# Optimization experiments

Measured on AMD Instinct MI355X. Metric: run time of the kernel, lower is better.

## Reference

```python
import jax, jax.numpy as jnp
import numpy as np

K = 10          # number of neighbors (init kwarg k)
NUM_CLASSES = 100  # label vocabulary (targets drawn in [0, 100))


def setup_inputs() -> dict:
    key = jax.random.key(0)
    k1, k2, k3 = jax.random.split(key, 3)
    X = jax.random.normal(k1, (1024, 512), dtype=jnp.float32)
    data = jax.random.normal(k2, (50000, 512), dtype=jnp.float32)
    targets = jax.random.randint(k3, (50000,), 0, NUM_CLASSES, dtype=jnp.int64)
    return {"X": X, "data": data, "targets": targets}


def reference(X, data, targets):
    # Pairwise L2 distance (p=2 path of the module), computed via the
    x2 = jnp.sum(X * X, axis=1, keepdims=True)              # [Q, 1]
    d2 = jnp.sum(data * data, axis=1)                        # [N]
    sq = x2 + d2[None, :] - 2.0 * (X @ data.T)               # [Q, N]
    dist = jnp.sqrt(jnp.maximum(sq, 0.0))                    # torch.norm(p1-p2, p=2)

    # torch: sort distances ascending, take first k indices -> top-k smallest.
    _, idx = jax.lax.top_k(-dist, K)                         # [Q, K]
    labels = targets[idx]                                    # [Q, K]

    # torch.mode over the k neighbor labels: histogram + argmax.
    # argmax picks the first (smallest) class on ties, matching torch.mode.
    counts = jax.nn.one_hot(labels, NUM_CLASSES, dtype=jnp.float32).sum(axis=1)  # [Q, C]
    pred = jnp.argmax(counts, axis=1).astype(jnp.float32)    # [Q]
    return pred
```

## Files before the change

kernel.cpp:

```cpp
#include <hip/hip_runtime.h>
#include <math.h>
#include <limits.h>

#define QN 1024
#define NN 50000
#define NPAD 50048
#define DD 512
#define KNN 10
#define NT 128
#define QTB 128
#define BK 32
#define NS 391
#define QB 8
#define NSAMP 31
#define NREST (NS - NSAMP)
#define CAP 512
#define SLACK 4.0f
#define LCAP 1152

#define WS_D2  0
#define WS_TAU 50048
#define WS_CNT (WS_TAU + 1024)
#define WS_XH  (WS_CNT + 1024)
#define WS_CKS (WS_XH + QN * DD / 2)
#define WS_BUF (WS_CKS + QN * NSAMP * KNN * 2)
#define WS_DH  (WS_BUF + QN * CAP * 2)
#define WS_END (WS_DH + NS * 16 * 2048)

typedef __attribute__((ext_vector_type(8))) short short8;
typedef __attribute__((ext_vector_type(4))) float f32x4;
typedef unsigned long long u64;

__device__ __forceinline__ u64 mkkey(float f, int idx) {
  unsigned u = __float_as_uint(f);
  unsigned m = u ^ ((unsigned)((int)u >> 31) | 0x80000000u);
  return ((u64)m << 32) | (unsigned)idx;
}

__device__ __forceinline__ float keyhi_f(unsigned m) {
  unsigned u = (m & 0x80000000u) ? (m ^ 0x80000000u) : ~m;
  return __uint_as_float(u);
}

__device__ __forceinline__ unsigned cvth(float x, float y) {
  unsigned ux = __float_as_uint(x), uy = __float_as_uint(y);
  unsigned rx = ux + 0x7fffu + ((ux >> 16) & 1u);
  unsigned ry = uy + 0x7fffu + ((uy >> 16) & 1u);
  return (rx >> 16) | (ry & 0xffff0000u);
}

__device__ __forceinline__ void glds16(const void* g, void* l) {
  __builtin_amdgcn_global_load_lds(
      (const __attribute__((address_space(1))) unsigned*)g,
      (__attribute__((address_space(3))) unsigned*)l, 16, 0, 0);
}

__device__ __forceinline__ void ins10(u64* kl, u64 k) {
#pragma unroll
  for (int u = 0; u < KNN; u++) {
    u64 lo = (k < kl[u]) ? k : kl[u];
    u64 hi = (k < kl[u]) ? kl[u] : k;
    kl[u] = lo; k = hi;
  }
}

__global__ __launch_bounds__(256) void conv_kernel(
    const float* __restrict__ dat, const float* __restrict__ Xm,
    float* __restrict__ ws) {
  if ((int)blockIdx.x >= NS) {
    const int g = ((int)blockIdx.x - NS) * 256 + threadIdx.x;
    const int b = g >> 10, kc = (g >> 6) & 15, l = g & 63;
    const int row = b * 16 + (l & 15);
    const int col = kc * 32 + (l >> 4) * 8;
    const float4* p = (const float4*)(Xm + (size_t)row * DD + col);
    float4 v0 = p[0], v1 = p[1];
    ((uint4*)(ws + WS_XH))[g] = make_uint4(
        cvth(v0.x, v0.y), cvth(v0.z, v0.w), cvth(v1.x, v1.y), cvth(v1.z, v1.w));
    return;
  }
  const int slice = blockIdx.x;
  const int t = threadIdx.x;
  const int row = t >> 1, h2 = t & 1;
  const int gr = slice * NT + row;
  const int r15 = row & 15;
  float s = 0.f;
#pragma unroll
  for (int kc8 = 0; kc8 < 8; kc8++) {
    const int kc = h2 * 8 + kc8;
    float4 v[8];
    if (gr < NN) {
      const float4* src = (const float4*)(dat + (size_t)gr * DD + kc * 32);
#pragma unroll
      for (int j = 0; j < 8; j++) v[j] = src[j];
    } else {
#pragma unroll
      for (int j = 0; j < 8; j++) v[j] = make_float4(0.f, 0.f, 0.f, 0.f);
    }
    unsigned hw[16];
#pragma unroll
    for (int j = 0; j < 8; j++) {
      s = fmaf(v[j].x, v[j].x, s); s = fmaf(v[j].y, v[j].y, s);
      s = fmaf(v[j].z, v[j].z, s); s = fmaf(v[j].w, v[j].w, s);
      hw[2 * j]     = cvth(v[j].x, v[j].y);
      hw[2 * j + 1] = cvth(v[j].z, v[j].w);
    }
    uint4* dhp = (uint4*)((unsigned char*)(ws + WS_DH) +
                          (((size_t)slice * 16 + kc) * 8 + (row >> 4)) * 1024);
#pragma unroll
    for (int qd = 0; qd < 4; qd++)
      dhp[qd * 16 + r15] = make_uint4(hw[4 * qd], hw[4 * qd + 1], hw[4 * qd + 2], hw[4 * qd + 3]);
  }
  s += __shfl_xor(s, 1, 64);
  if (h2 == 0) ws[WS_D2 + gr] = (gr < NN) ? s : __builtin_inff();
}

struct StageT { unsigned char ah[8192], bh[8192]; };
struct EpiT  { float sq[64][132]; };
struct ListT { u64 kl[64][4][KNN]; };

template <int MODE> struct SmemSel {
  union U { StageT s; EpiT e; ListT l; };
};
template <> struct SmemSel<1> {
  struct U { StageT s; float tau[128]; };
};

template <int PRE, int MODE>
__global__ __launch_bounds__(256, 3) void knn_chunk(
    const float* __restrict__ dat, float* __restrict__ ws, int soff) {
  __shared__ __align__(16) typename SmemSel<MODE>::U sm;
  int bqx, bsy;
  if (MODE == 1 && (gridDim.y & 7) == 0) {
    const int n = (int)(blockIdx.y * gridDim.x + blockIdx.x);
    const int m = n >> 3;
    const int ypx = (int)(gridDim.y >> 3);
    bqx = m & 7;
    bsy = (n & 7) * ypx + (m >> 3);
  } else {
    bqx = blockIdx.x; bsy = blockIdx.y;
  }
  const int qbase = bqx * QTB;
  const int slice = bsy + soff;
  const int nbase = slice * NT;
  const int t = threadIdx.x;
  const int lane = t & 63, wave = t >> 6;
  const int wn = wave & 1, wq = wave >> 1;
  const unsigned char* dh = (const unsigned char*)(ws + WS_DH);
  const char* xfh = (const char*)(ws + WS_XH);

  f32x4 acc[4][4];
#pragma unroll
  for (int i = 0; i < 4; i++)
#pragma unroll
    for (int j = 0; j < 4; j++) acc[i][j] = (f32x4)0.f;

  auto stage = [&](int kc) {
#pragma unroll
    for (int i = 0; i < 2; i++) {
      int pp = wave * 2 + i;
      const char* ga = xfh +
          ((((size_t)(bqx * 8 + pp) * 16 + kc) * 64) + lane) * 16;
      glds16(ga, sm.s.ah + pp * 1024);
    }
#pragma unroll
    for (int i = 0; i < 2; i++) {
      int p = wave * 2 + i;
      const unsigned char* gb = dh +
          (((size_t)slice * 16 + kc) * 8 + p) * 1024 + lane * 16;
      glds16(gb, sm.s.bh + p * 1024);
    }
  };

  if (PRE) {
    stage(0);
    for (int kc = 0; kc < 16; kc++) {
      __syncthreads();
      const int fragoff = lane * 16;
      short8 fah[4], fbh[4];
#pragma unroll
      for (int i = 0; i < 4; i++) {
        fah[i] = *(const short8*)(sm.s.ah + (wq * 4 + i) * 1024 + fragoff);
        fbh[i] = *(const short8*)(sm.s.bh + (wn * 4 + i) * 1024 + fragoff);
      }
      __syncthreads();
      if (kc < 15) stage(kc + 1);
#pragma unroll
      for (int mt = 0; mt < 4; mt++)
#pragma unroll
        for (int nt = 0; nt < 4; nt++)
          acc[mt][nt] = __builtin_amdgcn_mfma_f32_16x16x32_bf16(fah[mt], fbh[nt], acc[mt][nt], 0, 0, 0);
    }
  } else {
    const int abase = (((bqx * 8 + wq * 4) * 16) * 64 + lane) * 16;
    const int brow = t >> 1, bh_half = t & 1;
    const int bgr = nbase + brow;
    const int bpanel = (brow >> 4) * 1024;
    const int bchunk = (brow & 15) * 16;
    for (int kc = 0; kc < 16; kc++) {
      const int kk = kc * BK;
      short8 fah[4];
#pragma unroll
      for (int i = 0; i < 4; i++)
        fah[i] = *(const short8*)(xfh + abase + i * 16384 + kc * 1024);
      __syncthreads();
      {
        float4 v0 = make_float4(0.f, 0.f, 0.f, 0.f), v1 = v0, v2 = v0, v3 = v0;
        if (bgr < NN) {
          const float4* src = (const float4*)(dat + (size_t)bgr * DD + kk + bh_half * 16);
          v0 = src[0]; v1 = src[1]; v2 = src[2]; v3 = src[3];
        }
        unsigned char* bhp = sm.s.bh + bpanel;
        *(uint4*)(bhp + (2 * bh_half) * 256 + bchunk) =
            make_uint4(cvth(v0.x, v0.y), cvth(v0.z, v0.w), cvth(v1.x, v1.y), cvth(v1.z, v1.w));
        *(uint4*)(bhp + (2 * bh_half + 1) * 256 + bchunk) =
            make_uint4(cvth(v2.x, v2.y), cvth(v2.z, v2.w), cvth(v3.x, v3.y), cvth(v3.z, v3.w));
      }
      __syncthreads();
      const int fragoff = lane * 16;
      short8 fbh[4];
#pragma unroll
      for (int i = 0; i < 4; i++)
        fbh[i] = *(const short8*)(sm.s.bh + (wn * 4 + i) * 1024 + fragoff);
      __syncthreads();
#pragma unroll
      for (int mt = 0; mt < 4; mt++)
#pragma unroll
        for (int nt = 0; nt < 4; nt++)
          acc[mt][nt] = __builtin_amdgcn_mfma_f32_16x16x32_bf16(fah[mt], fbh[nt], acc[mt][nt], 0, 0, 0);
    }
  }

  if constexpr (MODE == 0) {
#pragma unroll
    for (int pass = 0; pass < 2; pass++) {
      __syncthreads();
      if (wq == pass) {
#pragma unroll
        for (int nt = 0; nt < 4; nt++) {
          int col = wn * 64 + nt * 16 + (lane & 15);
          float d2v = ws[WS_D2 + nbase + col];
#pragma unroll
          for (int mt = 0; mt < 4; mt++)
#pragma unroll
            for (int rg = 0; rg < 4; rg++) {
              int lr = mt * 16 + (lane >> 4) * 4 + rg;
              sm.e.sq[lr][col] = fmaf(-2.f, acc[mt][nt][rg], d2v);
            }
        }
      }
      __syncthreads();
      {
        const int r = t >> 2, s = t & 3;
        u64 kl[KNN];
#pragma unroll
        for (int u = 0; u < KNN; u++) kl[u] = ~0ull;
        for (int jj = 0; jj < 32; jj++) {
          int c = s * 32 + ((jj + r + 8 * s) & 31);
          float v = sm.e.sq[r][c];
          ins10(kl, mkkey(v, nbase + c));
        }
        __syncthreads();
#pragma unroll
        for (int u = 0; u < KNN; u++) sm.l.kl[r][s][u] = kl[u];
      }
      __syncthreads();
      if (t < 64) {
        u64* dst = ((u64*)(ws + WS_CKS)) +
                   ((size_t)(qbase + pass * 64 + t) * NSAMP + blockIdx.y) * KNN;
        int h0 = 0, h1 = 0, h2 = 0, h3 = 0;
        for (int pick = 0; pick < KNN; pick++) {
          u64 k0 = sm.l.kl[t][0][h0], k1 = sm.l.kl[t][1][h1];
          u64 k2 = sm.l.kl[t][2][h2], k3 = sm.l.kl[t][3][h3];
          u64 best = k0; int bm = 0;
          if (k1 < best) { best = k1; bm = 1; }
          if (k2 < best) { best = k2; bm = 2; }
          if (k3 < best) { best = k3; bm = 3; }
          dst[pick] = best;
          h0 += (bm == 0); h1 += (bm == 1); h2 += (bm == 2); h3 += (bm == 3);
        }
      }
    }
  } else {
    if (t < 128) sm.tau[t] = ws[WS_TAU + qbase + t];
    __syncthreads();
    unsigned* cnt = (unsigned*)(ws + WS_CNT);
    u64* buf = (u64*)(ws + WS_BUF);
    float d2v[4];
#pragma unroll
    for (int nt = 0; nt < 4; nt++)
      d2v[nt] = ws[WS_D2 + nbase + wn * 64 + nt * 16 + (lane & 15)];
#pragma unroll
    for (int mt = 0; mt < 4; mt++)
#pragma unroll
      for (int rg = 0; rg < 4; rg++) {
        int row = wq * 64 + mt * 16 + (lane >> 4) * 4 + rg;
        float tr = sm.tau[row];
#pragma unroll
        for (int nt = 0; nt < 4; nt++) {
          float d = fmaf(-2.f, acc[mt][nt][rg], d2v[nt]);
          if (d < tr) {
            int col = nbase + wn * 64 + nt * 16 + (lane & 15);
            int q = qbase + row;
            unsigned slot = atomicAdd(cnt + q, 1u);
            if (slot < CAP) buf[(size_t)q * CAP + slot] = mkkey(d, col);
          }
        }
      }
  }
}

__global__ __launch_bounds__(64) void tau_kernel(float* __restrict__ ws) {
  const int q = blockIdx.x;
  const int t = threadIdx.x;
  const u64* samp = ((const u64*)(ws + WS_CKS)) + (size_t)q * NSAMP * KNN;
  const int NC = NSAMP * KNN;
  u64 kl[KNN];
#pragma unroll
  for (int u = 0; u < KNN; u++) kl[u] = ~0ull;
  for (int j = t; j < NC; j += 64) ins10(kl, samp[j]);
  __shared__ u64 wk[64][KNN];
  __shared__ u64 m2[8][KNN];
#pragma unroll
  for (int u = 0; u < KNN; u++) wk[t][u] = kl[u];
  __syncthreads();
  if (t < 8) {
    int h[8] = {0, 0, 0, 0, 0, 0, 0, 0};
    for (int pick = 0; pick < KNN; pick++) {
      u64 best = ~0ull; int bm = 0;
#pragma unroll
      for (int m = 0; m < 8; m++) {
        u64 km = wk[t * 8 + m][h[m]];
        if (km < best) { best = km; bm = m; }
      }
      m2[t][pick] = best;
#pragma unroll
      for (int m = 0; m < 8; m++) h[m] += (bm == m);
    }
  }
  __syncthreads();
  if (t == 0) {
    int h[8] = {0, 0, 0, 0, 0, 0, 0, 0};
    u64 best = 0;
    for (int pick = 0; pick < KNN; pick++) {
      best = ~0ull; int bm = 0;
#pragma unroll
      for (int m = 0; m < 8; m++) {
        u64 km = m2[m][h[m]];
        if (km < best) { best = km; bm = m; }
      }
#pragma unroll
      for (int m = 0; m < 8; m++) h[m] += (bm == m);
    }
    ws[WS_TAU + q] = keyhi_f((unsigned)(best >> 32)) + SLACK;
    ((unsigned*)(ws + WS_CNT))[q] = 0u;
  }
}

__global__ __launch_bounds__(256) void knn_final(
    const int* __restrict__ targets, const float* __restrict__ Xm,
    const float* __restrict__ dat, float* __restrict__ ws,
    float* __restrict__ out) {
  const int q = blockIdx.x;
  const int t = threadIdx.x;
  const int lane = t & 63, wave = t >> 6;
  __shared__ float qrow[DD];
  __shared__ unsigned lst[LCAP];
  __shared__ int nlist;
  __shared__ u64 wk4[4][KNN];
  if (t == 0) nlist = 0;
  if (t < 128) ((float4*)qrow)[t] = ((const float4*)(Xm + (size_t)q * DD))[t];
  __syncthreads();
  const float tr = ws[WS_TAU + q];
  const u64* samp = ((const u64*)(ws + WS_CKS)) + (size_t)q * NSAMP * KNN;
  for (int j = t; j < NSAMP * KNN; j += 256) {
    u64 k = samp[j];
    if (keyhi_f((unsigned)(k >> 32)) < tr) {
      int s_ = atomicAdd(&nlist, 1);
      if (s_ < LCAP) lst[s_] = (unsigned)k;
    }
  }
  unsigned c = ((const unsigned*)(ws + WS_CNT))[q];
  if (c > CAP) c = CAP;
  const u64* buf = ((const u64*)(ws + WS_BUF)) + (size_t)q * CAP;
  for (int j = t; j < (int)c; j += 256) {
    int s_ = atomicAdd(&nlist, 1);
    if (s_ < LCAP) lst[s_] = (unsigned)buf[j];
  }
  __syncthreads();
  const int n = nlist < LCAP ? nlist : LCAP;

  u64 kl[KNN];
#pragma unroll
  for (int u = 0; u < KNN; u++) kl[u] = ~0ull;
  const float4* qv = (const float4*)qrow;
  const float4 q0 = qv[lane * 2], q1 = qv[lane * 2 + 1];
  for (int j = wave; j < n; j += 8) {
    const unsigned i0 = lst[j];
    const int has1 = (j + 4) < n;
    const unsigned i1 = has1 ? lst[j + 4] : i0;
    const float4* x0 = (const float4*)(dat + (size_t)i0 * DD) + lane * 2;
    const float4* x1 = (const float4*)(dat + (size_t)i1 * DD) + lane * 2;
    const float4 a0 = x0[0], a1 = x0[1];
    const float4 b0 = x1[0], b1 = x1[1];
    float p0 = a0.x * q0.x, p1 = b0.x * q0.x;
    p0 = fmaf(a0.y, q0.y, p0); p1 = fmaf(b0.y, q0.y, p1);
    p0 = fmaf(a0.z, q0.z, p0); p1 = fmaf(b0.z, q0.z, p1);
    p0 = fmaf(a0.w, q0.w, p0); p1 = fmaf(b0.w, q0.w, p1);
    p0 = fmaf(a1.x, q1.x, p0); p1 = fmaf(b1.x, q1.x, p1);
    p0 = fmaf(a1.y, q1.y, p0); p1 = fmaf(b1.y, q1.y, p1);
    p0 = fmaf(a1.z, q1.z, p0); p1 = fmaf(b1.z, q1.z, p1);
    p0 = fmaf(a1.w, q1.w, p0); p1 = fmaf(b1.w, q1.w, p1);
#pragma unroll
    for (int s_ = 1; s_ < 64; s_ <<= 1) {
      p0 += __shfl_xor(p0, s_, 64);
      p1 += __shfl_xor(p1, s_, 64);
    }
    float d0 = fmaf(-2.f, p0, ws[WS_D2 + i0]);
    u64 k0 = mkkey(d0, (int)i0);
    if (k0 < kl[KNN - 1]) ins10(kl, k0);
    if (has1) {
      float d1 = fmaf(-2.f, p1, ws[WS_D2 + i1]);
      u64 k1 = mkkey(d1, (int)i1);
      if (k1 < kl[KNN - 1]) ins10(kl, k1);
    }
  }
  if (lane == 0)
#pragma unroll
    for (int u = 0; u < KNN; u++) wk4[wave][u] = kl[u];
  __syncthreads();
  if (t == 0) {
    int h[4] = {0, 0, 0, 0};
    int fi[KNN];
    for (int pick = 0; pick < KNN; pick++) {
      u64 best = ~0ull; int bm = 0;
#pragma unroll
      for (int m = 0; m < 4; m++) {
        u64 km = wk4[m][h[m]];
        if (km < best) { best = km; bm = m; }
      }
      fi[pick] = (int)(unsigned)(best & 0xffffffffu);
      h[bm]++;
    }
    int lab[KNN];
#pragma unroll
    for (int u = 0; u < KNN; u++) lab[u] = targets[fi[u]];
    int bc = 0, bl = INT_MAX;
#pragma unroll
    for (int i = 0; i < KNN; i++) {
      int cc = 0;
#pragma unroll
      for (int j = 0; j < KNN; j++) cc += (lab[j] == lab[i]) ? 1 : 0;
      if (cc > bc || (cc == bc && lab[i] < bl)) { bc = cc; bl = lab[i]; }
    }
    out[q] = (float)bl;
  }
}

extern "C" void kernel_launch(void* const* d_in, const int* in_sizes, int n_in,
                              void* d_out, int out_size, void* d_ws, size_t ws_size,
                              hipStream_t stream) {
  const float* Xm  = (const float*)d_in[0];
  const float* dat = (const float*)d_in[1];
  const int* targets = (const int*)d_in[2];
  float* out = (float*)d_out;
  float* ws  = (float*)d_ws;
  const bool pre = ws_size >= (size_t)WS_END * 4;

  hipLaunchKernelGGL(conv_kernel, dim3(NS + QN * DD / 8 / 256), dim3(256), 0,
                     stream, dat, Xm, ws);
  if (pre) {
    hipLaunchKernelGGL((knn_chunk<1, 0>), dim3(QB, NSAMP), dim3(256), 0, stream, dat, ws, 0);
    hipLaunchKernelGGL(tau_kernel, dim3(QN), dim3(64), 0, stream, ws);
    hipLaunchKernelGGL((knn_chunk<1, 1>), dim3(QB, NREST), dim3(256), 0, stream, dat, ws, NSAMP);
  } else {
    hipLaunchKernelGGL((knn_chunk<0, 0>), dim3(QB, NSAMP), dim3(256), 0, stream, dat, ws, 0);
    hipLaunchKernelGGL(tau_kernel, dim3(QN), dim3(64), 0, stream, ws);
    hipLaunchKernelGGL((knn_chunk<0, 1>), dim3(QB, NREST), dim3(256), 0, stream, dat, ws, NSAMP);
  }
  hipLaunchKernelGGL(knn_final, dim3(QN), dim3(256), 0, stream, targets, Xm, dat, ws, out);
}
```

Baseline: 335.2 us.

## Fuse conversion and sample top-k into one kernel, enlarge sample set

Merges the fp32-to-bf16 conversion kernel and the sampling top-k kernel into one launch. The sampling blocks now load fp32 data directly, convert X and data in registers and compute norms inline, while the other blocks convert only the remaining slices. The sample slice count doubles from 31 to 63 to tighten the threshold for the filter pass. The workspace-size fallback path is dropped, so the large workspace is always assumed. The cost is more sample-phase work and uncoalesced fp32 reads of X in the sampling blocks, in exchange for one fewer launch and a tighter threshold that should mean fewer filter candidates.

```diff
diff --git a/kernel.cpp b/kernel.cpp
--- a/kernel.cpp
+++ b/kernel.cpp
@@ -12,7 +12,7 @@
 #define BK 32
 #define NS 391
 #define QB 8
-#define NSAMP 31
+#define NSAMP 63
 #define NREST (NS - NSAMP)
 #define CAP 512
 #define SLACK 4.0f
@@ -64,11 +64,21 @@
   }
 }
 
-__global__ __launch_bounds__(256) void conv_kernel(
+struct EpiT  { float sq[64][132]; };
+struct ListT { u64 kl[64][4][KNN]; };
+struct Smem0 {
+  union { unsigned char bh[8192]; EpiT e; ListT l; } u;
+  float d2loc[128];
+};
+
+__global__ __launch_bounds__(256, 3) void fused_kernel(
     const float* __restrict__ dat, const float* __restrict__ Xm,
     float* __restrict__ ws) {
-  if ((int)blockIdx.x >= NS) {
-    const int g = ((int)blockIdx.x - NS) * 256 + threadIdx.x;
+  const int bid = (int)blockIdx.x;
+  const int t = threadIdx.x;
+
+  if (bid >= QB * NSAMP + NREST) {
+    const int g = (bid - (QB * NSAMP + NREST)) * 256 + t;
     const int b = g >> 10, kc = (g >> 6) & 15, l = g & 63;
     const int row = b * 16 + (l & 15);
     const int col = kc * 32 + (l >> 4) * 8;
@@ -78,75 +88,189 @@
         cvth(v0.x, v0.y), cvth(v0.z, v0.w), cvth(v1.x, v1.y), cvth(v1.z, v1.w));
     return;
   }
-  const int slice = blockIdx.x;
-  const int t = threadIdx.x;
-  const int row = t >> 1, h2 = t & 1;
-  const int gr = slice * NT + row;
-  const int r15 = row & 15;
+
+  if (bid >= QB * NSAMP) {
+    const int slice = NSAMP + (bid - QB * NSAMP);
+    const int row = t >> 1, h2 = t & 1;
+    const int gr = slice * NT + row;
+    const int r15 = row & 15;
+    float s = 0.f;
+#pragma unroll
+    for (int kc8 = 0; kc8 < 8; kc8++) {
+      const int kc = h2 * 8 + kc8;
+      float4 v[8];
+      if (gr < NN) {
+        const float4* src = (const float4*)(dat + (size_t)gr * DD + kc * 32);
+#pragma unroll
+        for (int j = 0; j < 8; j++) v[j] = src[j];
+      } else {
+#pragma unroll
+        for (int j = 0; j < 8; j++) v[j] = make_float4(0.f, 0.f, 0.f, 0.f);
+      }
+      unsigned hw[16];
+#pragma unroll
+      for (int j = 0; j < 8; j++) {
+        s = fmaf(v[j].x, v[j].x, s); s = fmaf(v[j].y, v[j].y, s);
+        s = fmaf(v[j].z, v[j].z, s); s = fmaf(v[j].w, v[j].w, s);
+        hw[2 * j]     = cvth(v[j].x, v[j].y);
+        hw[2 * j + 1] = cvth(v[j].z, v[j].w);
+      }
+      uint4* dhp = (uint4*)((unsigned char*)(ws + WS_DH) +
+                            (((size_t)slice * 16 + kc) * 8 + (row >> 4)) * 1024);
+#pragma unroll
+      for (int qd = 0; qd < 4; qd++)
+        dhp[qd * 16 + r15] = make_uint4(hw[4 * qd], hw[4 * qd + 1], hw[4 * qd + 2], hw[4 * qd + 3]);
+    }
+    s += __shfl_xor(s, 1, 64);
+    if (h2 == 0) ws[WS_D2 + gr] = (gr < NN) ? s : __builtin_inff();
+    return;
+  }
+
+  __shared__ __align__(16) Smem0 sm;
+  const int m = bid;
+  const int bqx = m & 7;
+  const int bsy = m >> 3;
+  const int qbase = bqx * QTB;
+  const int slice = bsy;
+  const int nbase = slice * NT;
+  const int lane = t & 63, wave = t >> 6;
+  const int wn = wave & 1, wq = wave >> 1;
+
+  f32x4 acc[4][4];
+#pragma unroll
+  for (int i = 0; i < 4; i++)
+#pragma unroll
+    for (int j = 0; j < 4; j++) acc[i][j] = (f32x4)0.f;
+
+  const int brow = t >> 1, bh_half = t & 1;
+  const int bgr = nbase + brow;
+  const int bpanel = (brow >> 4) * 1024;
+  const int bchunk = (brow & 15) * 16;
   float s = 0.f;
-#pragma unroll
-  for (int kc8 = 0; kc8 < 8; kc8++) {
-    const int kc = h2 * 8 + kc8;
-    float4 v[8];
-    if (gr < NN) {
-      const float4* src = (const float4*)(dat + (size_t)gr * DD + kc * 32);
-#pragma unroll
-      for (int j = 0; j < 8; j++) v[j] = src[j];
-    } else {
-#pragma unroll
-      for (int j = 0; j < 8; j++) v[j] = make_float4(0.f, 0.f, 0.f, 0.f);
-    }
-    unsigned hw[16];
-#pragma unroll
-    for (int j = 0; j < 8; j++) {
-      s = fmaf(v[j].x, v[j].x, s); s = fmaf(v[j].y, v[j].y, s);
-      s = fmaf(v[j].z, v[j].z, s); s = fmaf(v[j].w, v[j].w, s);
-      hw[2 * j]     = cvth(v[j].x, v[j].y);
-      hw[2 * j + 1] = cvth(v[j].z, v[j].w);
-    }
-    uint4* dhp = (uint4*)((unsigned char*)(ws + WS_DH) +
-                          (((size_t)slice * 16 + kc) * 8 + (row >> 4)) * 1024);
-#pragma unroll
-    for (int qd = 0; qd < 4; qd++)
-      dhp[qd * 16 + r15] = make_uint4(hw[4 * qd], hw[4 * qd + 1], hw[4 * qd + 2], hw[4 * qd + 3]);
+  for (int kc = 0; kc < 16; kc++) {
+    const int kk = kc * BK;
+    short8 fah[4];
+#pragma unroll
+    for (int i = 0; i < 4; i++) {
+      const int p = wq * 4 + i;
+      const float4* xr = (const float4*)(
+          Xm + (size_t)(qbase + p * 16 + (lane & 15)) * DD + kk + (lane >> 4) * 8);
+      float4 v0 = xr[0], v1 = xr[1];
+      union { unsigned w[4]; short8 s8; } pk;
+      pk.w[0] = cvth(v0.x, v0.y); pk.w[1] = cvth(v0.z, v0.w);
+      pk.w[2] = cvth(v1.x, v1.y); pk.w[3] = cvth(v1.z, v1.w);
+      fah[i] = pk.s8;
+    }
+    __syncthreads();
+    {
+      float4 v0 = make_float4(0.f, 0.f, 0.f, 0.f), v1 = v0, v2 = v0, v3 = v0;
+      if (bgr < NN) {
+        const float4* src = (const float4*)(dat + (size_t)bgr * DD + kk + bh_half * 16);
+        v0 = src[0]; v1 = src[1]; v2 = src[2]; v3 = src[3];
+      }
+      s = fmaf(v0.x, v0.x, s); s = fmaf(v0.y, v0.y, s);
+      s = fmaf(v0.z, v0.z, s); s = fmaf(v0.w, v0.w, s);
+      s = fmaf(v1.x, v1.x, s); s = fmaf(v1.y, v1.y, s);
+      s = fmaf(v1.z, v1.z, s); s = fmaf(v1.w, v1.w, s);
+      s = fmaf(v2.x, v2.x, s); s = fmaf(v2.y, v2.y, s);
+      s = fmaf(v2.z, v2.z, s); s = fmaf(v2.w, v2.w, s);
+      s = fmaf(v3.x, v3.x, s); s = fmaf(v3.y, v3.y, s);
+      s = fmaf(v3.z, v3.z, s); s = fmaf(v3.w, v3.w, s);
+      uint4 q0 = make_uint4(cvth(v0.x, v0.y), cvth(v0.z, v0.w), cvth(v1.x, v1.y), cvth(v1.z, v1.w));
+      uint4 q1 = make_uint4(cvth(v2.x, v2.y), cvth(v2.z, v2.w), cvth(v3.x, v3.y), cvth(v3.z, v3.w));
+      unsigned char* bhp = sm.u.bh + bpanel;
+      *(uint4*)(bhp + (2 * bh_half) * 256 + bchunk)     = q0;
+      *(uint4*)(bhp + (2 * bh_half + 1) * 256 + bchunk) = q1;
+    }
+    __syncthreads();
+    const int fragoff = lane * 16;
+    short8 fbh[4];
+#pragma unroll
+    for (int i = 0; i < 4; i++)
+      fbh[i] = *(const short8*)(sm.u.bh + (wn * 4 + i) * 1024 + fragoff);
+    __syncthreads();
+#pragma unroll
+    for (int mt = 0; mt < 4; mt++)
+#pragma unroll
+      for (int nt = 0; nt < 4; nt++)
+        acc[mt][nt] = __builtin_amdgcn_mfma_f32_16x16x32_bf16(fah[mt], fbh[nt], acc[mt][nt], 0, 0, 0);
   }
   s += __shfl_xor(s, 1, 64);
-  if (h2 == 0) ws[WS_D2 + gr] = (gr < NN) ? s : __builtin_inff();
-}
-
-struct StageT { unsigned char ah[8192], bh[8192]; };
-struct EpiT  { float sq[64][132]; };
-struct ListT { u64 kl[64][4][KNN]; };
-
-template <int MODE> struct SmemSel {
-  union U { StageT s; EpiT e; ListT l; };
-};
-template <> struct SmemSel<1> {
-  struct U { StageT s; float tau[128]; };
-};
-
-template <int PRE, int MODE>
-__global__ __launch_bounds__(256, 3) void knn_chunk(
-    const float* __restrict__ dat, float* __restrict__ ws, int soff) {
-  __shared__ __align__(16) typename SmemSel<MODE>::U sm;
-  int bqx, bsy;
-  if (MODE == 1 && (gridDim.y & 7) == 0) {
-    const int n = (int)(blockIdx.y * gridDim.x + blockIdx.x);
-    const int m = n >> 3;
-    const int ypx = (int)(gridDim.y >> 3);
-    bqx = m & 7;
-    bsy = (n & 7) * ypx + (m >> 3);
-  } else {
-    bqx = blockIdx.x; bsy = blockIdx.y;
-  }
+  if (bh_half == 0) {
+    sm.d2loc[brow] = s;
+    ws[WS_D2 + bgr] = s;
+  }
+
+#pragma unroll
+  for (int pass = 0; pass < 2; pass++) {
+    __syncthreads();
+    if (wq == pass) {
+#pragma unroll
+      for (int nt = 0; nt < 4; nt++) {
+        int col = wn * 64 + nt * 16 + (lane & 15);
+        float d2v = sm.d2loc[col];
+#pragma unroll
+        for (int mt = 0; mt < 4; mt++)
+#pragma unroll
+          for (int rg = 0; rg < 4; rg++) {
+            int lr = mt * 16 + (lane >> 4) * 4 + rg;
+            sm.u.e.sq[lr][col] = fmaf(-2.f, acc[mt][nt][rg], d2v);
+          }
+      }
+    }
+    __syncthreads();
+    {
+      const int r = t >> 2, s4 = t & 3;
+      u64 kl[KNN];
+#pragma unroll
+      for (int u = 0; u < KNN; u++) kl[u] = ~0ull;
+      for (int jj = 0; jj < 32; jj++) {
+        int c = s4 * 32 + ((jj + r + 8 * s4) & 31);
+        float v = sm.u.e.sq[r][c];
+        ins10(kl, mkkey(v, nbase + c));
+      }
+      __syncthreads();
+#pragma unroll
+      for (int u = 0; u < KNN; u++) sm.u.l.kl[r][s4][u] = kl[u];
+    }
+    __syncthreads();
+    if (t < 64) {
+      u64* dst = ((u64*)(ws + WS_CKS)) +
+                 ((size_t)(qbase + pass * 64 + t) * NSAMP + bsy) * KNN;
+      int h0 = 0, h1 = 0, h2c = 0, h3 = 0;
+      for (int pick = 0; pick < KNN; pick++) {
+        u64 k0 = sm.u.l.kl[t][0][h0], k1 = sm.u.l.kl[t][1][h1];
+        u64 k2 = sm.u.l.kl[t][2][h2c], k3 = sm.u.l.kl[t][3][h3];
+        u64 best = k0; int bm = 0;
+        if (k1 < best) { best = k1; bm = 1; }
+        if (k2 < best) { best = k2; bm = 2; }
+        if (k3 < best) { best = k3; bm = 3; }
+        dst[pick] = best;
+        h0 += (bm == 0); h1 += (bm == 1); h2c += (bm == 2); h3 += (bm == 3);
+      }
+    }
+  }
+}
+
+struct SmemF { unsigned char bh[8192]; float tau[128]; };
+
+__global__ __launch_bounds__(256, 3) void knn_filter(
+    float* __restrict__ ws) {
+  __shared__ __align__(16) SmemF sm;
+  const int n = (int)(blockIdx.y * gridDim.x + blockIdx.x);
+  const int mm = n >> 3;
+  const int ypx = (int)(gridDim.y >> 3);
+  const int bqx = mm & 7;
+  const int bsy = (n & 7) * ypx + (mm >> 3);
   const int qbase = bqx * QTB;
-  const int slice = bsy + soff;
+  const int slice = bsy + NSAMP;
   const int nbase = slice * NT;
   const int t = threadIdx.x;
   const int lane = t & 63, wave = t >> 6;
   const int wn = wave & 1, wq = wave >> 1;
   const unsigned char* dh = (const unsigned char*)(ws + WS_DH);
   const char* xfh = (const char*)(ws + WS_XH);
+  const int abase = (((bqx * 8 + wq * 4) * 16) * 64 + lane) * 16;
 
   f32x4 acc[4][4];
 #pragma unroll
@@ -154,159 +278,62 @@
 #pragma unroll
     for (int j = 0; j < 4; j++) acc[i][j] = (f32x4)0.f;
 
-  auto stage = [&](int kc) {
-#pragma unroll
-    for (int i = 0; i < 2; i++) {
-      int pp = wave * 2 + i;
-      const char* ga = xfh +
-          ((((size_t)(bqx * 8 + pp) * 16 + kc) * 64) + lane) * 16;
-      glds16(ga, sm.s.ah + pp * 1024);
-    }
+  auto stageB = [&](int kc) {
 #pragma unroll
     for (int i = 0; i < 2; i++) {
       int p = wave * 2 + i;
-      const unsigned char* gb = dh +
+      const unsigned char* g = dh +
           (((size_t)slice * 16 + kc) * 8 + p) * 1024 + lane * 16;
-      glds16(gb, sm.s.bh + p * 1024);
+      glds16(g, sm.bh + p * 1024);
     }
   };
 
-  if (PRE) {
-    stage(0);
-    for (int kc = 0; kc < 16; kc++) {
-      __syncthreads();
-      const int fragoff = lane * 16;
-      short8 fah[4], fbh[4];
-#pragma unroll
-      for (int i = 0; i < 4; i++) {
-        fah[i] = *(const short8*)(sm.s.ah + (wq * 4 + i) * 1024 + fragoff);
-        fbh[i] = *(const short8*)(sm.s.bh + (wn * 4 + i) * 1024 + fragoff);
-      }
-      __syncthreads();
-      if (kc < 15) stage(kc + 1);
-#pragma unroll
-      for (int mt = 0; mt < 4; mt++)
-#pragma unroll
-        for (int nt = 0; nt < 4; nt++)
-          acc[mt][nt] = __builtin_amdgcn_mfma_f32_16x16x32_bf16(fah[mt], fbh[nt], acc[mt][nt], 0, 0, 0);
-    }
-  } else {
-    const int abase = (((bqx * 8 + wq * 4) * 16) * 64 + lane) * 16;
-    const int brow = t >> 1, bh_half = t & 1;
-    const int bgr = nbase + brow;
-    const int bpanel = (brow >> 4) * 1024;
-    const int bchunk = (brow & 15) * 16;
-    for (int kc = 0; kc < 16; kc++) {
-      const int kk = kc * BK;
-      short8 fah[4];
-#pragma unroll
-      for (int i = 0; i < 4; i++)
-        fah[i] = *(const short8*)(xfh + abase + i * 16384 + kc * 1024);
-      __syncthreads();
-      {
-        float4 v0 = make_float4(0.f, 0.f, 0.f, 0.f), v1 = v0, v2 = v0, v3 = v0;
-        if (bgr < NN) {
-          const float4* src = (const float4*)(dat + (size_t)bgr * DD + kk + bh_half * 16);
-          v0 = src[0]; v1 = src[1]; v2 = src[2]; v3 = src[3];
+  stageB(0);
+  for (int kc = 0; kc < 16; kc++) {
+    short8 fah[4];
+#pragma unroll
+    for (int i = 0; i < 4; i++)
+      fah[i] = *(const short8*)(xfh + abase + i * 16384 + kc * 1024);
+    __syncthreads();
+    const int fragoff = lane * 16;
+    short8 fbh[4];
+#pragma unroll
+    for (int i = 0; i < 4; i++)
+      fbh[i] = *(const short8*)(sm.bh + (wn * 4 + i) * 1024 + fragoff);
+    __syncthreads();
+    if (kc < 15) stageB(kc + 1);
+#pragma unroll
+    for (int mt = 0; mt < 4; mt++)
+#pragma unroll
+      for (int nt = 0; nt < 4; nt++)
+        acc[mt][nt] = __builtin_amdgcn_mfma_f32_16x16x32_bf16(fah[mt], fbh[nt], acc[mt][nt], 0, 0, 0);
+  }
+
+  if (t < 128) sm.tau[t] = ws[WS_TAU + qbase + t];
+  __syncthreads();
+  unsigned* cnt = (unsigned*)(ws + WS_CNT);
+  u64* buf = (u64*)(ws + WS_BUF);
+  float d2v[4];
+#pragma unroll
+  for (int nt = 0; nt < 4; nt++)
+    d2v[nt] = ws[WS_D2 + nbase + wn * 64 + nt * 16 + (lane & 15)];
+#pragma unroll
+  for (int mt = 0; mt < 4; mt++)
+#pragma unroll
+    for (int rg = 0; rg < 4; rg++) {
+      int row = wq * 64 + mt * 16 + (lane >> 4) * 4 + rg;
+      float tr = sm.tau[row];
+#pragma unroll
+      for (int nt = 0; nt < 4; nt++) {
+        float d = fmaf(-2.f, acc[mt][nt][rg], d2v[nt]);
+        if (d < tr) {
+          int col = nbase + wn * 64 + nt * 16 + (lane & 15);
+          int q = qbase + row;
+          unsigned slot = atomicAdd(cnt + q, 1u);
+          if (slot < CAP) buf[(size_t)q * CAP + slot] = mkkey(d, col);
         }
-        unsigned char* bhp = sm.s.bh + bpanel;
-        *(uint4*)(bhp + (2 * bh_half) * 256 + bchunk) =
-            make_uint4(cvth(v0.x, v0.y), cvth(v0.z, v0.w), cvth(v1.x, v1.y), cvth(v1.z, v1.w));
-        *(uint4*)(bhp + (2 * bh_half + 1) * 256 + bchunk) =
-            make_uint4(cvth(v2.x, v2.y), cvth(v2.z, v2.w), cvth(v3.x, v3.y), cvth(v3.z, v3.w));
-      }
-      __syncthreads();
-      const int fragoff = lane * 16;
-      short8 fbh[4];
-#pragma unroll
-      for (int i = 0; i < 4; i++)
-        fbh[i] = *(const short8*)(sm.s.bh + (wn * 4 + i) * 1024 + fragoff);
-      __syncthreads();
-#pragma unroll
-      for (int mt = 0; mt < 4; mt++)
-#pragma unroll
-        for (int nt = 0; nt < 4; nt++)
-          acc[mt][nt] = __builtin_amdgcn_mfma_f32_16x16x32_bf16(fah[mt], fbh[nt], acc[mt][nt], 0, 0, 0);
-    }
-  }
-
-  if constexpr (MODE == 0) {
-#pragma unroll
-    for (int pass = 0; pass < 2; pass++) {
-      __syncthreads();
-      if (wq == pass) {
-#pragma unroll
-        for (int nt = 0; nt < 4; nt++) {
-          int col = wn * 64 + nt * 16 + (lane & 15);
-          float d2v = ws[WS_D2 + nbase + col];
-#pragma unroll
-          for (int mt = 0; mt < 4; mt++)
-#pragma unroll
-            for (int rg = 0; rg < 4; rg++) {
-              int lr = mt * 16 + (lane >> 4) * 4 + rg;
-              sm.e.sq[lr][col] = fmaf(-2.f, acc[mt][nt][rg], d2v);
-            }
-        }
-      }
-      __syncthreads();
-      {
-        const int r = t >> 2, s = t & 3;
-        u64 kl[KNN];
-#pragma unroll
-        for (int u = 0; u < KNN; u++) kl[u] = ~0ull;
-        for (int jj = 0; jj < 32; jj++) {
-          int c = s * 32 + ((jj + r + 8 * s) & 31);
-          float v = sm.e.sq[r][c];
-          ins10(kl, mkkey(v, nbase + c));
-        }
-        __syncthreads();
-#pragma unroll
-        for (int u = 0; u < KNN; u++) sm.l.kl[r][s][u] = kl[u];
-      }
-      __syncthreads();
-      if (t < 64) {
-        u64* dst = ((u64*)(ws + WS_CKS)) +
-                   ((size_t)(qbase + pass * 64 + t) * NSAMP + blockIdx.y) * KNN;
-        int h0 = 0, h1 = 0, h2 = 0, h3 = 0;
-        for (int pick = 0; pick < KNN; pick++) {
-          u64 k0 = sm.l.kl[t][0][h0], k1 = sm.l.kl[t][1][h1];
-          u64 k2 = sm.l.kl[t][2][h2], k3 = sm.l.kl[t][3][h3];
-          u64 best = k0; int bm = 0;
-          if (k1 < best) { best = k1; bm = 1; }
-          if (k2 < best) { best = k2; bm = 2; }
-          if (k3 < best) { best = k3; bm = 3; }
-          dst[pick] = best;
-          h0 += (bm == 0); h1 += (bm == 1); h2 += (bm == 2); h3 += (bm == 3);
-        }
-      }
-    }
-  } else {
-    if (t < 128) sm.tau[t] = ws[WS_TAU + qbase + t];
-    __syncthreads();
-    unsigned* cnt = (unsigned*)(ws + WS_CNT);
-    u64* buf = (u64*)(ws + WS_BUF);
-    float d2v[4];
-#pragma unroll
-    for (int nt = 0; nt < 4; nt++)
-      d2v[nt] = ws[WS_D2 + nbase + wn * 64 + nt * 16 + (lane & 15)];
-#pragma unroll
-    for (int mt = 0; mt < 4; mt++)
-#pragma unroll
-      for (int rg = 0; rg < 4; rg++) {
-        int row = wq * 64 + mt * 16 + (lane >> 4) * 4 + rg;
-        float tr = sm.tau[row];
-#pragma unroll
-        for (int nt = 0; nt < 4; nt++) {
-          float d = fmaf(-2.f, acc[mt][nt][rg], d2v[nt]);
-          if (d < tr) {
-            int col = nbase + wn * 64 + nt * 16 + (lane & 15);
-            int q = qbase + row;
-            unsigned slot = atomicAdd(cnt + q, 1u);
-            if (slot < CAP) buf[(size_t)q * CAP + slot] = mkkey(d, col);
-          }
-        }
-      }
-  }
+      }
+    }
 }
 
 __global__ __launch_bounds__(64) void tau_kernel(float* __restrict__ ws) {
@@ -464,18 +491,10 @@
   const int* targets = (const int*)d_in[2];
   float* out = (float*)d_out;
   float* ws  = (float*)d_ws;
-  const bool pre = ws_size >= (size_t)WS_END * 4;
-
-  hipLaunchKernelGGL(conv_kernel, dim3(NS + QN * DD / 8 / 256), dim3(256), 0,
+
+  hipLaunchKernelGGL(fused_kernel, dim3(QB * NSAMP + NREST + 256), dim3(256), 0,
                      stream, dat, Xm, ws);
-  if (pre) {
-    hipLaunchKernelGGL((knn_chunk<1, 0>), dim3(QB, NSAMP), dim3(256), 0, stream, dat, ws, 0);
-    hipLaunchKernelGGL(tau_kernel, dim3(QN), dim3(64), 0, stream, ws);
-    hipLaunchKernelGGL((knn_chunk<1, 1>), dim3(QB, NREST), dim3(256), 0, stream, dat, ws, NSAMP);
-  } else {
-    hipLaunchKernelGGL((knn_chunk<0, 0>), dim3(QB, NSAMP), dim3(256), 0, stream, dat, ws, 0);
-    hipLaunchKernelGGL(tau_kernel, dim3(QN), dim3(64), 0, stream, ws);
-    hipLaunchKernelGGL((knn_chunk<0, 1>), dim3(QB, NREST), dim3(256), 0, stream, dat, ws, NSAMP);
-  }
+  hipLaunchKernelGGL(tau_kernel, dim3(QN), dim3(64), 0, stream, ws);
+  hipLaunchKernelGGL(knn_filter, dim3(QB, NREST), dim3(256), 0, stream, ws);
   hipLaunchKernelGGL(knn_final, dim3(QN), dim3(256), 0, stream, targets, Xm, dat, ws, out);
 }
```

Measured after the change: 331.9 us. No clear change (-1.0%).
